# Kernel tuning notes

Hardware: AMD Instinct MI355X
Metric: run time of the kernel (lower is better)

Reference implementation:

```python
import jax, jax.numpy as jnp
import numpy as np

B, N, K, D, H, L = 2, 2048, 256, 768, 150, 11
REL_PROP = 2
NB = 10  # distance buckets


def _lin(key, din, dout):
    return jax.random.normal(key, (din, dout), dtype=jnp.float32) / np.sqrt(din)


def setup_inputs() -> dict:
    key = jax.random.key(0)
    ks = jax.random.split(key, 16)
    rng = np.random.default_rng(0)
    prune_idx = jnp.asarray(np.stack([np.sort(rng.permutation(N)[:K]) for _ in range(B)]), dtype=jnp.int32)
    span_begin = jnp.sort(jax.random.randint(ks[2], (B, K), 0, N - 16), axis=-1).astype(jnp.int32)
    span_end = (span_begin + jax.random.randint(ks[3], (B, K), 1, 16)).astype(jnp.int32)
    return {
        "all_span_vecs": jax.random.normal(ks[0], (B, N, D), dtype=jnp.float32),
        "update": jax.random.normal(ks[1], (B, K, D), dtype=jnp.float32),
        "square_mask": jnp.ones((B, K, K), dtype=jnp.float32),
        "span_lengths": jnp.full((B,), float(K), dtype=jnp.float32),
        "span_begin": span_begin,
        "span_end": span_end,
        "prune_indices": prune_idx,
        "w_left": _lin(ks[4], D, H), "b_left": jnp.zeros((H,), jnp.float32),
        "w_right": _lin(ks[5], D, H), "b_right": jnp.zeros((H,), jnp.float32),
        "dist_emb": jax.random.normal(ks[6], (NB, H), dtype=jnp.float32) * 0.02,
        "w_h": _lin(ks[7], H, H), "b_h": jnp.zeros((H,), jnp.float32),
        "w_out": _lin(ks[8], H, L), "b_out": jnp.zeros((L,), jnp.float32),
        "a_w": _lin(ks[9], L, D),
        "gate_w": _lin(ks[10], 2 * D, D), "gate_b": jnp.zeros((D,), jnp.float32),
        "pr_w": _lin(ks[11], D, 1), "pr_b": jnp.zeros((1,), jnp.float32),
    }


def _pair_scores(u, bins, w_left, b_left, w_right, b_right, dist_emb, w_h, b_h, w_out, b_out):
    # OptFFpairs: left/right span projections + pairwise distance embedding -> FF -> L labels
    left = u @ w_left + b_left          # [B,K,H]
    right = u @ w_right + b_right       # [B,K,H]
    h = jax.nn.relu(left[:, :, None, :] + right[:, None, :, :] + dist_emb[bins])  # [B,K,K,H]
    h = jax.nn.relu(h @ w_h + b_h)
    return h @ w_out + b_out            # [B,K,K,L]


def _add_unary(rel, ss):
    # relation_add_scores: add per-span pruner scores along both pair axes; ss: [B,K,1]
    return rel + ss[:, :, None, :] + ss[:, None, :, :]


def reference(all_span_vecs, update, square_mask, span_lengths, span_begin, span_end,
              prune_indices, w_left, b_left, w_right, b_right, dist_emb, w_h, b_h,
              w_out, b_out, a_w, gate_w, gate_b, pr_w, pr_b):
    bins = jnp.clip(jnp.abs(span_begin[:, None, :] - span_begin[:, :, None]), 0, NB - 1)  # [B,K,K]
    rel = _pair_scores(update, bins, w_left, b_left, w_right, b_right, dist_emb, w_h, b_h, w_out, b_out)
    rel = _add_unary(rel, update @ pr_w + pr_b)
    for _ in range(REL_PROP):
        probs = jax.nn.relu(rel) * square_mask[..., None]     # [B,K,K,L]
        msg = probs @ a_w                                     # A(probs): [B,K,K,D]
        # ctxt[b,j,d] = sum_i msg[b,i,j,d] * update[b,i,d] / span_lengths[b]
        ctxt = (msg * update[:, :, None, :]).sum(-3) / span_lengths[:, None, None]
        g = jax.nn.sigmoid(jnp.concatenate([update, ctxt], axis=-1) @ gate_w + gate_b)
        update = g * update + (1.0 - g) * ctxt                # MyGate
        rel = _pair_scores(update, bins, w_left, b_left, w_right, b_right, dist_emb, w_h, b_h, w_out, b_out)
        rel = _add_unary(rel, update @ pr_w + pr_b)           # pruner.scorer(update)
    # overwrite_spans: scatter updated filtered spans back into the full span tensor
    valid = jnp.arange(K)[None, :] < span_lengths[:, None]    # [B,K]
    bidx = jnp.arange(B)[:, None]
    orig = all_span_vecs[bidx, prune_indices]                 # [B,K,D]
    vals = jnp.where(valid[..., None], update, orig)
    update_all = all_span_vecs.at[bidx, prune_indices].set(vals)
    return update_all, update, rel
```

## Files before the change

kernel.cpp:

```cpp
#include <hip/hip_runtime.h>
#include <hip/hip_bf16.h>
#include <math.h>

#define BB 2
#define NN 2048
#define KK 256
#define DD 768
#define HH 150
#define LL 11
#define NBINS 10

#define KP 160
#define WP 40
#define GWP 136
#define BPAD 264

typedef __attribute__((ext_vector_type(8))) short short8;
typedef __attribute__((ext_vector_type(4))) short s16x4;
typedef __attribute__((ext_vector_type(4))) float f32x4;

__device__ inline unsigned bf2u(float lo, float hi) {
  union { __hip_bfloat162 b; unsigned u; } cv;
  cv.b = __float22bfloat162_rn(make_float2(lo, hi));
  return cv.u;
}
__device__ inline short bf1(float x) {
  union { __hip_bfloat16 b; short s; } cv;
  cv.b = __float2bfloat16(x);
  return cv.s;
}
__device__ inline float ubf(short b) {
  return __uint_as_float(((unsigned)(unsigned short)b) << 16);
}

#define PRE_PREP 110
#define PRE_CVT  1536
#define PRE_TRGW 1152
#define PRE_TRWLR 240
#define PRE_TRUPD 384
#define PRE_NB (PRE_PREP + PRE_CVT + PRE_TRGW + PRE_TRWLR + PRE_TRUPD)

__global__ __launch_bounds__(256) void k_pre(
    const float* __restrict__ w_h, const float* __restrict__ w_out,
    short* __restrict__ wt, short* __restrict__ wo,
    const float* __restrict__ upd_in, short* __restrict__ updbf,
    const float* __restrict__ gate_w, short* __restrict__ gwt,
    const float* __restrict__ w_left, const float* __restrict__ w_right,
    short* __restrict__ wlrt, short* __restrict__ updT)
{
  __shared__ float tile[32][33];
  int bid = blockIdx.x;
  int t = threadIdx.x;

  if (bid < PRE_PREP) {
    int idx = bid * 256 + t;
    if (idx < KP * KP) {
      int n = idx / KP, k = idx - n * KP;
      float v = (n < HH && k < HH) ? w_h[k * HH + n] : 0.f;
      wt[idx] = bf1(v);
    }
    int idx2 = idx - KP * KP;
    if (idx2 >= 0 && idx2 < 16 * KP) {
      int n = idx2 / KP, k = idx2 - n * KP;
      float v = (n < LL && k < HH) ? w_out[k * LL + n] : 0.f;
      wo[idx2] = bf1(v);
    }
    return;
  }
  bid -= PRE_PREP;
  if (bid < PRE_CVT) {
    int idx = bid * 256 + t;
    if (idx < BB * KK * DD) updbf[idx] = bf1(upd_in[idx]);
    return;
  }
  bid -= PRE_CVT;
  if (bid < PRE_TRGW) {
    int kt = bid % 48, nt = bid / 48;
    int m0 = kt * 32, n0 = nt * 32;
    int tx = t & 31, ty = t >> 5;
    #pragma unroll
    for (int r = 0; r < 4; ++r)
      tile[ty + r * 8][tx] = gate_w[(size_t)(m0 + ty + r * 8) * DD + n0 + tx];
    __syncthreads();
    #pragma unroll
    for (int r = 0; r < 4; ++r)
      gwt[(size_t)(n0 + ty + r * 8) * (2 * DD) + m0 + tx] = bf1(tile[tx][ty + r * 8]);
    return;
  }
  bid -= PRE_TRGW;
  if (bid < PRE_TRWLR) {
    int kt = bid % 24, nt = bid / 24;
    int k0 = kt * 32, n0 = nt * 32;
    const float* src = (n0 >= KP) ? w_right : w_left;
    int col0 = n0 - (n0 >= KP ? KP : 0);
    int tx = t & 31, ty = t >> 5;
    #pragma unroll
    for (int r = 0; r < 4; ++r) {
      int col = col0 + tx;
      tile[ty + r * 8][tx] = (col < HH) ? src[(size_t)(k0 + ty + r * 8) * HH + col] : 0.f;
    }
    __syncthreads();
    #pragma unroll
    for (int r = 0; r < 4; ++r)
      wlrt[(size_t)(n0 + ty + r * 8) * DD + k0 + tx] = bf1(tile[tx][ty + r * 8]);
    return;
  }
  bid -= PRE_TRWLR;
  {
    int b = bid / 192;
    int r = bid - b * 192;
    int it = r & 7, dt = r >> 3;
    int i0 = it * 32, d0 = dt * 32;
    int tx = t & 31, ty = t >> 5;
    #pragma unroll
    for (int rr = 0; rr < 4; ++rr)
      tile[ty + rr * 8][tx] = upd_in[(size_t)(b * KK + i0 + ty + rr * 8) * DD + d0 + tx];
    __syncthreads();
    #pragma unroll
    for (int rr = 0; rr < 4; ++rr)
      updT[(size_t)(b * DD + d0 + ty + rr * 8) * KK + i0 + tx] = bf1(tile[tx][ty + rr * 8]);
  }
}

__global__ __launch_bounds__(256) void k_projss(
    const short* __restrict__ updbf, const short* __restrict__ wlrt,
    const float* __restrict__ b_left, const float* __restrict__ b_right,
    const float* __restrict__ updf, const float* __restrict__ pr_w,
    const float* __restrict__ pr_b,
    float* __restrict__ left, float* __restrict__ right, float* __restrict__ ssv)
{
  __shared__ short As[64][WP];
  __shared__ short Bs[KP][WP];
  int bidx = blockIdx.x;
  int t = threadIdx.x;

  if (bidx >= 16) {
    int row = (bidx - 16) * 4 + (t >> 6);
    int l = t & 63;
    float s = 0.f;
    for (int d = l; d < DD; d += 64) s = fmaf(updf[(size_t)row * DD + d], pr_w[d], s);
    #pragma unroll
    for (int off = 32; off > 0; off >>= 1) s += __shfl_down(s, off);
    if (l == 0) ssv[row] = s + pr_b[0];
    return;
  }

  int rbk = bidx >> 1, half = bidx & 1;
  int row0 = rbk * 64;
  const short* wsrc = wlrt + (size_t)half * KP * DD;
  int l = t & 63, w = t >> 6, lr = l & 15, lg = l >> 4;
  int ar = t >> 2, ac = t & 3;
  int i1 = t + 256, i2 = t + 512;
  f32x4 acc[10];
  #pragma unroll
  for (int nt = 0; nt < 10; ++nt) acc[nt] = (f32x4){0.f, 0.f, 0.f, 0.f};

  short8 pa, pb0, pb1, pb2 = {};
  pa  = *(const short8*)(updbf + (size_t)(row0 + ar) * DD + ac * 8);
  pb0 = *(const short8*)(wsrc + (size_t)(t >> 2) * DD + (t & 3) * 8);
  pb1 = *(const short8*)(wsrc + (size_t)(i1 >> 2) * DD + (i1 & 3) * 8);
  if (i2 < 640) pb2 = *(const short8*)(wsrc + (size_t)(i2 >> 2) * DD + (i2 & 3) * 8);

  for (int ks = 0; ks < 24; ++ks) {
    __syncthreads();
    *(short8*)&As[ar][ac * 8] = pa;
    *(short8*)&Bs[t >> 2][(t & 3) * 8] = pb0;
    *(short8*)&Bs[i1 >> 2][(i1 & 3) * 8] = pb1;
    if (i2 < 640) *(short8*)&Bs[i2 >> 2][(i2 & 3) * 8] = pb2;
    __syncthreads();
    if (ks + 1 < 24) {
      int k0 = (ks + 1) * 32;
      pa  = *(const short8*)(updbf + (size_t)(row0 + ar) * DD + k0 + ac * 8);
      pb0 = *(const short8*)(wsrc + (size_t)(t >> 2) * DD + k0 + (t & 3) * 8);
      pb1 = *(const short8*)(wsrc + (size_t)(i1 >> 2) * DD + k0 + (i1 & 3) * 8);
      if (i2 < 640) pb2 = *(const short8*)(wsrc + (size_t)(i2 >> 2) * DD + k0 + (i2 & 3) * 8);
    }
    short8 a = *(short8*)&As[w * 16 + lr][lg * 8];
    #pragma unroll
    for (int nt = 0; nt < 10; ++nt) {
      short8 b = *(short8*)&Bs[nt * 16 + lr][lg * 8];
      acc[nt] = __builtin_amdgcn_mfma_f32_16x16x32_bf16(a, b, acc[nt], 0, 0, 0);
    }
  }
  const float* bias = half ? b_right : b_left;
  float* dst = half ? right : left;
  int rowb = row0 + w * 16 + lg * 4;
  #pragma unroll
  for (int nt = 0; nt < 10; ++nt) {
    int col = nt * 16 + lr;
    if (col < HH) {
      float bv = bias[col];
      #pragma unroll
      for (int q = 0; q < 4; ++q)
        dst[(size_t)(rowb + q) * HH + col] = acc[nt][q] + bv;
    }
  }
}

template <bool WPT>
__global__ __launch_bounds__(256, 4) void k_pair_mfma(
    const float* __restrict__ left, const float* __restrict__ right,
    const float* __restrict__ ss, const int* __restrict__ span_begin,
    const float* __restrict__ demb,
    const short* __restrict__ wt, const short* __restrict__ wo,
    const float* __restrict__ b_h, const float* __restrict__ b_out,
    const float* __restrict__ mask,
    float* __restrict__ rel, short* __restrict__ probsT)
{
  int bid = blockIdx.x;
  int b  = bid >> 10;
  int r2 = bid & 1023;
  int i  = r2 >> 2;
  int j0 = (r2 & 3) * 64;

  __shared__ short wtbuf[2][32 * KP];
  __shared__ float ld_s[NBINS][KP];
  __shared__ float bh_s[KP];
  __shared__ float ssj_s[64];
  __shared__ float m_s[64];
  __shared__ int   bins[64];

  int t = threadIdx.x;
  int l = t & 63, w = t >> 6;
  int lr = l & 15, lg = l >> 4;

  int sbi = span_begin[b * KK + i];
  if (t < 64) {
    int d = span_begin[b * KK + j0 + t] - sbi; d = d < 0 ? -d : d;
    bins[t] = d > NBINS - 1 ? NBINS - 1 : d;
    ssj_s[t] = ss[b * KK + j0 + t];
    if (WPT) m_s[t] = mask[((size_t)(b * KK + i)) * KK + j0 + t];
  }
  for (int idx = t; idx < KP; idx += 256) bh_s[idx] = (idx < HH) ? b_h[idx] : 0.f;
  {
    const float* lrow = left + (size_t)(b * KK + i) * HH;
    for (int idx = t; idx < NBINS * KP; idx += 256) {
      int bn = idx / KP, k = idx - bn * KP;
      ld_s[bn][k] = (k < HH) ? (lrow[k] + demb[bn * HH + k]) : 0.f;
    }
  }
  short8 wo_f[5];
  #pragma unroll
  for (int ks = 0; ks < 5; ++ks)
    wo_f[ks] = *(const short8*)(wo + lr * KP + ks * 32 + lg * 8);

  short8 pw[3];
  #pragma unroll
  for (int c = 0; c < 3; ++c) {
    int idx = t + c * 256;
    if (idx < 640) pw[c] = *(const short8*)(wt + idx * 8);
  }
  #pragma unroll
  for (int c = 0; c < 3; ++c) {
    int idx = t + c * 256;
    if (idx < 640) *(short8*)&wtbuf[0][idx * 8] = pw[c];
  }
  #pragma unroll
  for (int c = 0; c < 3; ++c) {
    int idx = t + c * 256;
    if (idx < 640) pw[c] = *(const short8*)(wt + 5120 + idx * 8);
  }
  __syncthreads();

  int jr = w * 16 + lr;
  int binr = bins[jr];
  const float* rrow = right + (size_t)(b * KK + j0 + jr) * HH;
  const float* ldr = &ld_s[binr][0];
  short8 afr[5];
  #pragma unroll
  for (int ks = 0; ks < 5; ++ks) {
    unsigned pk[4];
    #pragma unroll
    for (int e = 0; e < 4; ++e) {
      int k = ks * 32 + lg * 8 + e * 2;
      float2 r2v = (k < HH - 1) ? *(const float2*)(rrow + k) : make_float2(0.f, 0.f);
      float2 lv = *(const float2*)(ldr + k);
      float v0 = fmaxf(lv.x + r2v.x, 0.f);
      float v1 = fmaxf(lv.y + r2v.y, 0.f);
      pk[e] = bf2u(v0, v1);
    }
    int4 tmp; tmp.x = (int)pk[0]; tmp.y = (int)pk[1]; tmp.z = (int)pk[2]; tmp.w = (int)pk[3];
    afr[ks] = *(short8*)&tmp;
  }

  f32x4 acc[10];
  #pragma unroll
  for (int m = 0; m < 10; ++m) acc[m] = (f32x4){0.f, 0.f, 0.f, 0.f};

  #pragma unroll
  for (int s = 0; s < 5; ++s) {
    if (s > 0) __syncthreads();
    if (s + 1 < 5) {
      #pragma unroll
      for (int c = 0; c < 3; ++c) {
        int idx = t + c * 256;
        if (idx < 640) *(short8*)&wtbuf[(s + 1) & 1][idx * 8] = pw[c];
      }
      if (s + 2 < 5) {
        #pragma unroll
        for (int c = 0; c < 3; ++c) {
          int idx = t + c * 256;
          if (idx < 640) pw[c] = *(const short8*)(wt + (s + 2) * 5120 + idx * 8);
        }
      }
    }
    const short* bufp = &wtbuf[s & 1][0];
    #pragma unroll
    for (int ks = 0; ks < 5; ++ks) {
      short8 a = afr[ks];
      #pragma unroll
      for (int ntp = 0; ntp < 2; ++ntp) {
        short8 bf = *(const short8*)(bufp + (ntp * 16 + lr) * KP + ks * 32 + lg * 8);
        acc[s * 2 + ntp] = __builtin_amdgcn_mfma_f32_16x16x32_bf16(a, bf, acc[s * 2 + ntp], 0, 0, 0);
      }
    }
  }
  __syncthreads();

  short* h1 = &wtbuf[0][0];
  #pragma unroll
  for (int m = 0; m < 10; ++m) {
    int col = (m >> 1) * 32 + (m & 1) * 16 + lr;
    float bh = bh_s[col];
    #pragma unroll
    for (int q = 0; q < 4; ++q) {
      int row = w * 16 + lg * 4 + q;
      h1[row * KP + col] = bf1(fmaxf(acc[m][q] + bh, 0.f));
    }
  }
  __syncthreads();

  f32x4 acc2 = (f32x4){0.f, 0.f, 0.f, 0.f};
  #pragma unroll
  for (int ks = 0; ks < 5; ++ks) {
    short8 a = *(const short8*)(h1 + (w * 16 + lr) * KP + ks * 32 + lg * 8);
    acc2 = __builtin_amdgcn_mfma_f32_16x16x32_bf16(a, wo_f[ks], acc2, 0, 0, 0);
  }

  float ssi = ss[b * KK + i];
  float* out_s = (float*)&ld_s[0][0];
  if (lr < LL) {
    float bo = b_out[lr];
    #pragma unroll
    for (int q = 0; q < 4; ++q) {
      int row = w * 16 + lg * 4 + q;
      out_s[row * 12 + lr] = acc2[q] + bo + ssi + ssj_s[row];
    }
  }
  __syncthreads();
  size_t base = ((size_t)(b * KK + i) * KK + j0) * LL;
  for (int idx = t; idx < 64 * LL; idx += 256) {
    int j = idx / LL, ll2 = idx - j * LL;
    rel[base + idx] = out_s[j * 12 + ll2];
  }
  if (WPT) {
    for (int idx = t; idx < 64 * LL; idx += 256) {
      int j = idx / LL, ll2 = idx - j * LL;
      float v = fmaxf(out_s[j * 12 + ll2], 0.f) * m_s[j];
      probsT[(((size_t)(b * LL + ll2)) * KK + j0 + j) * KK + i] = bf1(v);
    }
  }
}

__global__ __launch_bounds__(256) void k_ctxt_mfma(
    const short* __restrict__ probsT, const short* __restrict__ updT,
    const float* __restrict__ a_w, const float* __restrict__ span_len,
    short* __restrict__ ctxbf)
{
  int bidx = blockIdx.x;
  int b = bidx / 96;
  int r = bidx - b * 96;
  int jt = r / 12, dt = r - jt * 12;
  int j0 = jt * 32, d0 = dt * 64;

  __shared__ short Bs[64][BPAD];
  __shared__ short As[32][BPAD];

  int t = threadIdx.x, l = t & 63, w = t >> 6, lr = l & 15, lg = l >> 4;
  int wr = w >> 1, wc = w & 1;

  for (int s = 0; s < 8; ++s) {
    int idx = t + s * 256;
    int row = idx >> 5, c = idx & 31;
    *(short8*)&Bs[row][c * 8] =
        *(const short8*)(updT + ((size_t)(b * DD + d0 + row)) * KK + c * 8);
  }

  short8 pa[4];
  #pragma unroll
  for (int s = 0; s < 4; ++s) {
    int idx = t + s * 256;
    int row = idx >> 5, c = idx & 31;
    pa[s] = *(const short8*)(probsT + (((size_t)(b * LL + 0)) * KK + j0 + row) * KK + c * 8);
  }

  f32x4 accF[2];
  accF[0] = (f32x4){0.f, 0.f, 0.f, 0.f};
  accF[1] = (f32x4){0.f, 0.f, 0.f, 0.f};

  for (int ll = 0; ll < LL; ++ll) {
    __syncthreads();
    #pragma unroll
    for (int s = 0; s < 4; ++s) {
      int idx = t + s * 256;
      int row = idx >> 5, c = idx & 31;
      *(short8*)&As[row][c * 8] = pa[s];
    }
    if (ll + 1 < LL) {
      #pragma unroll
      for (int s = 0; s < 4; ++s) {
        int idx = t + s * 256;
        int row = idx >> 5, c = idx & 31;
        pa[s] = *(const short8*)(probsT + (((size_t)(b * LL + ll + 1)) * KK + j0 + row) * KK + c * 8);
      }
    }
    float awl[2];
    #pragma unroll
    for (int nt = 0; nt < 2; ++nt) awl[nt] = a_w[ll * DD + d0 + wc * 32 + nt * 16 + lr];
    __syncthreads();

    f32x4 accL[2];
    accL[0] = (f32x4){0.f, 0.f, 0.f, 0.f};
    accL[1] = (f32x4){0.f, 0.f, 0.f, 0.f};
    #pragma unroll
    for (int ks = 0; ks < 8; ++ks) {
      short8 a = *(short8*)&As[wr * 16 + lr][ks * 32 + lg * 8];
      #pragma unroll
      for (int nt = 0; nt < 2; ++nt) {
        short8 bf = *(short8*)&Bs[wc * 32 + nt * 16 + lr][ks * 32 + lg * 8];
        accL[nt] = __builtin_amdgcn_mfma_f32_16x16x32_bf16(a, bf, accL[nt], 0, 0, 0);
      }
    }
    #pragma unroll
    for (int nt = 0; nt < 2; ++nt)
      #pragma unroll
      for (int q = 0; q < 4; ++q)
        accF[nt][q] = fmaf(awl[nt], accL[nt][q], accF[nt][q]);
  }

  float inv = 1.f / span_len[b];
  int rowb = j0 + wr * 16 + lg * 4;
  #pragma unroll
  for (int nt = 0; nt < 2; ++nt) {
    int col = d0 + wc * 32 + nt * 16 + lr;
    #pragma unroll
    for (int q = 0; q < 4; ++q) {
      size_t off = (size_t)(b * KK + rowb + q) * DD + col;
      ctxbf[off] = bf1(accF[nt][q] * inv);
    }
  }
}

template <bool LAST>
__global__ __launch_bounds__(256) void k_gate_mfma(
    const short* __restrict__ updbf, const short* __restrict__ ctxbf,
    const short* __restrict__ gwt, const float* __restrict__ gate_b,
    const float* __restrict__ updr, float* __restrict__ updw,
    short* __restrict__ nxtbf, short* __restrict__ updT,
    const int* __restrict__ prune, const float* __restrict__ span_len,
    float* __restrict__ out_all)
{
  int rb = blockIdx.x / 12, cb = blockIdx.x - rb * 12;
  int row0 = rb * 32, col0 = cb * 64;
  __shared__ short As[32][GWP];
  __shared__ short Bs[64][GWP];
  int t = threadIdx.x, l = t & 63, w = t >> 6, lr = l & 15, lg = l >> 4;
  int wr = w >> 1, wc = w & 1;

  f32x4 acc[2];
  acc[0] = (f32x4){0.f, 0.f, 0.f, 0.f};
  acc[1] = (f32x4){0.f, 0.f, 0.f, 0.f};

  short8 pa[2], pb[4];
  #pragma unroll
  for (int s = 0; s < 2; ++s) {
    int idx = t + s * 256;
    pa[s] = *(const short8*)(updbf + (size_t)(row0 + (idx >> 4)) * DD + (idx & 15) * 8);
  }
  #pragma unroll
  for (int s = 0; s < 4; ++s) {
    int idx = t + s * 256;
    pb[s] = *(const short8*)(gwt + (size_t)(col0 + (idx >> 4)) * (2 * DD) + (idx & 15) * 8);
  }

  for (int ph = 0; ph < 12; ++ph) {
    __syncthreads();
    #pragma unroll
    for (int s = 0; s < 2; ++s) {
      int idx = t + s * 256;
      *(short8*)&As[idx >> 4][(idx & 15) * 8] = pa[s];
    }
    #pragma unroll
    for (int s = 0; s < 4; ++s) {
      int idx = t + s * 256;
      *(short8*)&Bs[idx >> 4][(idx & 15) * 8] = pb[s];
    }
    if (ph + 1 < 12) {
      int k0 = (ph + 1) * 128;
      #pragma unroll
      for (int s = 0; s < 2; ++s) {
        int idx = t + s * 256;
        int ka = k0 + (idx & 15) * 8;
        const short* asrc = (ka < DD) ? (updbf + (size_t)(row0 + (idx >> 4)) * DD + ka)
                                      : (ctxbf + (size_t)(row0 + (idx >> 4)) * DD + ka - DD);
        pa[s] = *(const short8*)asrc;
      }
      #pragma unroll
      for (int s = 0; s < 4; ++s) {
        int idx = t + s * 256;
        pb[s] = *(const short8*)(gwt + (size_t)(col0 + (idx >> 4)) * (2 * DD) + k0 + (idx & 15) * 8);
      }
    }
    __syncthreads();
    #pragma unroll
    for (int ksub = 0; ksub < 4; ++ksub) {
      short8 a = *(short8*)&As[wr * 16 + lr][ksub * 32 + lg * 8];
      #pragma unroll
      for (int nt = 0; nt < 2; ++nt) {
        short8 bf = *(short8*)&Bs[wc * 32 + nt * 16 + lr][ksub * 32 + lg * 8];
        acc[nt] = __builtin_amdgcn_mfma_f32_16x16x32_bf16(a, bf, acc[nt], 0, 0, 0);
      }
    }
  }
  int rowb = row0 + wr * 16 + lg * 4;
  int bb = rowb >> 8, ii = rowb & 255;
  #pragma unroll
  for (int nt = 0; nt < 2; ++nt) {
    int col = col0 + wc * 32 + nt * 16 + lr;
    float gb = gate_b[col];
    s16x4 tw;
    #pragma unroll
    for (int q = 0; q < 4; ++q) {
      size_t off = (size_t)(rowb + q) * DD + col;
      float x = acc[nt][q] + gb;
      float g = 1.f / (1.f + expf(-x));
      float cv = ubf(ctxbf[off]);
      float o = g * updr[off] + (1.f - g) * cv;
      updw[off] = o;
      short bv = bf1(o);
      nxtbf[off] = bv;
      tw[q] = bv;
      if (LAST) {
        int iq = ii + q;
        if ((float)iq < span_len[bb]) {
          int dst = prune[bb * KK + iq];
          out_all[((size_t)(bb * NN + dst)) * DD + col] = o;
        }
      }
    }
    *(s16x4*)(updT + ((size_t)(bb * DD + col)) * KK + ii) = tw;
  }
}

extern "C" void kernel_launch(void* const* d_in, const int* in_sizes, int n_in,
                              void* d_out, int out_size, void* d_ws, size_t ws_size,
                              hipStream_t stream)
{
  (void)in_sizes; (void)n_in; (void)out_size; (void)ws_size;
  const float* all_span = (const float*)d_in[0];
  const float* upd_in   = (const float*)d_in[1];
  const float* mask     = (const float*)d_in[2];
  const float* span_len = (const float*)d_in[3];
  const int*   span_beg = (const int*)d_in[4];
  const int*   prune    = (const int*)d_in[6];
  const float* w_left   = (const float*)d_in[7];
  const float* b_left   = (const float*)d_in[8];
  const float* w_right  = (const float*)d_in[9];
  const float* b_right  = (const float*)d_in[10];
  const float* dist_emb = (const float*)d_in[11];
  const float* w_h      = (const float*)d_in[12];
  const float* b_h      = (const float*)d_in[13];
  const float* w_out    = (const float*)d_in[14];
  const float* b_out    = (const float*)d_in[15];
  const float* a_w      = (const float*)d_in[16];
  const float* gate_w   = (const float*)d_in[17];
  const float* gate_b   = (const float*)d_in[18];
  const float* pr_w     = (const float*)d_in[19];
  const float* pr_b     = (const float*)d_in[20];

  float* out_all = (float*)d_out;
  float* out_upd = out_all + (size_t)BB * NN * DD;
  float* out_rel = out_upd + (size_t)BB * KK * DD;

  float* ws     = (float*)d_ws;
  float* left   = ws;
  float* right  = left + (size_t)BB * KK * HH;
  float* ssv    = right + (size_t)BB * KK * HH + 64;
  short* wt_bf  = (short*)(ssv + (size_t)BB * KK);
  short* wo_bf  = wt_bf + KP * KP;
  short* updbf0 = wo_bf + 16 * KP;
  short* updbf1 = updbf0 + (size_t)BB * KK * DD;
  short* ctxbf  = updbf1 + (size_t)BB * KK * DD;
  short* gwt    = ctxbf + (size_t)BB * KK * DD;
  short* wlrt   = gwt + (size_t)DD * 2 * DD;
  short* probsT = wlrt + (size_t)2 * KP * DD;
  short* updT   = probsT + (size_t)BB * LL * KK * KK;

  hipMemcpyAsync(out_all, all_span, sizeof(float) * (size_t)BB * NN * DD,
                 hipMemcpyDeviceToDevice, stream);
  k_pre<<<PRE_NB, 256, 0, stream>>>(w_h, w_out, wt_bf, wo_bf, upd_in, updbf0,
                                    gate_w, gwt, w_left, w_right, wlrt, updT);

  k_projss<<<144, 256, 0, stream>>>(updbf0, wlrt, b_left, b_right, upd_in,
                                    pr_w, pr_b, left, right, ssv);
  k_pair_mfma<true><<<BB * KK * 4, 256, 0, stream>>>(
      left, right, ssv, span_beg, dist_emb, wt_bf, wo_bf, b_h, b_out, mask,
      out_rel, probsT);

  for (int p = 0; p < 2; ++p) {
    short* cur_bf = (p == 0) ? updbf0 : updbf1;
    short* nxt_bf = (p == 0) ? updbf1 : updbf0;
    const float* updr = (p == 0) ? upd_in : out_upd;
    k_ctxt_mfma<<<BB * 8 * 12, 256, 0, stream>>>(probsT, updT, a_w, span_len, ctxbf);
    if (p == 0) {
      k_gate_mfma<false><<<16 * 12, 256, 0, stream>>>(
          cur_bf, ctxbf, gwt, gate_b, updr, out_upd, nxt_bf, updT,
          prune, span_len, out_all);
    } else {
      k_gate_mfma<true><<<16 * 12, 256, 0, stream>>>(
          cur_bf, ctxbf, gwt, gate_b, updr, out_upd, nxt_bf, updT,
          prune, span_len, out_all);
    }
    k_projss<<<144, 256, 0, stream>>>(nxt_bf, wlrt, b_left, b_right, out_upd,
                                      pr_w, pr_b, left, right, ssv);
    if (p == 0) {
      k_pair_mfma<true><<<BB * KK * 4, 256, 0, stream>>>(
          left, right, ssv, span_beg, dist_emb, wt_bf, wo_bf, b_h, b_out, mask,
          out_rel, probsT);
    } else {
      k_pair_mfma<false><<<BB * KK * 4, 256, 0, stream>>>(
          left, right, ssv, span_beg, dist_emb, wt_bf, wo_bf, b_h, b_out, mask,
          out_rel, probsT);
    }
  }
}
```

Baseline: 190.7 us.

## Vectorize bf16 convert, skip dead rel writes, halve ctxt tile width

```diff
diff --git a/kernel.cpp b/kernel.cpp
--- a/kernel.cpp
+++ b/kernel.cpp
@@ -34,7 +34,7 @@
 }
 
 #define PRE_PREP 110
-#define PRE_CVT  1536
+#define PRE_CVT  192
 #define PRE_TRGW 1152
 #define PRE_TRWLR 240
 #define PRE_TRUPD 384
@@ -69,8 +69,15 @@
   }
   bid -= PRE_PREP;
   if (bid < PRE_CVT) {
-    int idx = bid * 256 + t;
-    if (idx < BB * KK * DD) updbf[idx] = bf1(upd_in[idx]);
+    int idx = (bid * 256 + t) * 8;
+    const float4* s4 = (const float4*)(upd_in + idx);
+    float4 a = s4[0], c = s4[1];
+    int4 pk;
+    pk.x = (int)bf2u(a.x, a.y);
+    pk.y = (int)bf2u(a.z, a.w);
+    pk.z = (int)bf2u(c.x, c.y);
+    pk.w = (int)bf2u(c.z, c.w);
+    *(int4*)(updbf + idx) = pk;
     return;
   }
   bid -= PRE_CVT;
@@ -348,12 +355,13 @@
     }
   }
   __syncthreads();
-  size_t base = ((size_t)(b * KK + i) * KK + j0) * LL;
-  for (int idx = t; idx < 64 * LL; idx += 256) {
-    int j = idx / LL, ll2 = idx - j * LL;
-    rel[base + idx] = out_s[j * 12 + ll2];
-  }
-  if (WPT) {
+  if (!WPT) {
+    size_t base = ((size_t)(b * KK + i) * KK + j0) * LL;
+    for (int idx = t; idx < 64 * LL; idx += 256) {
+      int j = idx / LL, ll2 = idx - j * LL;
+      rel[base + idx] = out_s[j * 12 + ll2];
+    }
+  } else {
     for (int idx = t; idx < 64 * LL; idx += 256) {
       int j = idx / LL, ll2 = idx - j * LL;
       float v = fmaxf(out_s[j * 12 + ll2], 0.f) * m_s[j];
@@ -368,18 +376,18 @@
     short* __restrict__ ctxbf)
 {
   int bidx = blockIdx.x;
-  int b = bidx / 96;
-  int r = bidx - b * 96;
-  int jt = r / 12, dt = r - jt * 12;
-  int j0 = jt * 32, d0 = dt * 64;
-
-  __shared__ short Bs[64][BPAD];
+  int b = bidx / 192;
+  int r = bidx - b * 192;
+  int jt = r / 24, dt = r - jt * 24;
+  int j0 = jt * 32, d0 = dt * 32;
+
+  __shared__ short Bs[32][BPAD];
   __shared__ short As[32][BPAD];
 
   int t = threadIdx.x, l = t & 63, w = t >> 6, lr = l & 15, lg = l >> 4;
   int wr = w >> 1, wc = w & 1;
 
-  for (int s = 0; s < 8; ++s) {
+  for (int s = 0; s < 4; ++s) {
     int idx = t + s * 256;
     int row = idx >> 5, c = idx & 31;
     *(short8*)&Bs[row][c * 8] =
@@ -394,9 +402,7 @@
     pa[s] = *(const short8*)(probsT + (((size_t)(b * LL + 0)) * KK + j0 + row) * KK + c * 8);
   }
 
-  f32x4 accF[2];
-  accF[0] = (f32x4){0.f, 0.f, 0.f, 0.f};
-  accF[1] = (f32x4){0.f, 0.f, 0.f, 0.f};
+  f32x4 accF = (f32x4){0.f, 0.f, 0.f, 0.f};
 
   for (int ll = 0; ll < LL; ++ll) {
     __syncthreads();
@@ -414,40 +420,28 @@
         pa[s] = *(const short8*)(probsT + (((size_t)(b * LL + ll + 1)) * KK + j0 + row) * KK + c * 8);
       }
     }
-    float awl[2];
-    #pragma unroll
-    for (int nt = 0; nt < 2; ++nt) awl[nt] = a_w[ll * DD + d0 + wc * 32 + nt * 16 + lr];
-    __syncthreads();
-
-    f32x4 accL[2];
-    accL[0] = (f32x4){0.f, 0.f, 0.f, 0.f};
-    accL[1] = (f32x4){0.f, 0.f, 0.f, 0.f};
+    float awl = a_w[ll * DD + d0 + wc * 16 + lr];
+    __syncthreads();
+
+    f32x4 accL = (f32x4){0.f, 0.f, 0.f, 0.f};
     #pragma unroll
     for (int ks = 0; ks < 8; ++ks) {
       short8 a = *(short8*)&As[wr * 16 + lr][ks * 32 + lg * 8];
-      #pragma unroll
-      for (int nt = 0; nt < 2; ++nt) {
-        short8 bf = *(short8*)&Bs[wc * 32 + nt * 16 + lr][ks * 32 + lg * 8];
-        accL[nt] = __builtin_amdgcn_mfma_f32_16x16x32_bf16(a, bf, accL[nt], 0, 0, 0);
-      }
-    }
-    #pragma unroll
-    for (int nt = 0; nt < 2; ++nt)
-      #pragma unroll
-      for (int q = 0; q < 4; ++q)
-        accF[nt][q] = fmaf(awl[nt], accL[nt][q], accF[nt][q]);
+      short8 bf = *(short8*)&Bs[wc * 16 + lr][ks * 32 + lg * 8];
+      accL = __builtin_amdgcn_mfma_f32_16x16x32_bf16(a, bf, accL, 0, 0, 0);
+    }
+    #pragma unroll
+    for (int q = 0; q < 4; ++q)
+      accF[q] = fmaf(awl, accL[q], accF[q]);
   }
 
   float inv = 1.f / span_len[b];
   int rowb = j0 + wr * 16 + lg * 4;
-  #pragma unroll
-  for (int nt = 0; nt < 2; ++nt) {
-    int col = d0 + wc * 32 + nt * 16 + lr;
-    #pragma unroll
-    for (int q = 0; q < 4; ++q) {
-      size_t off = (size_t)(b * KK + rowb + q) * DD + col;
-      ctxbf[off] = bf1(accF[nt][q] * inv);
-    }
+  int col = d0 + wc * 16 + lr;
+  #pragma unroll
+  for (int q = 0; q < 4; ++q) {
+    size_t off = (size_t)(b * KK + rowb + q) * DD + col;
+    ctxbf[off] = bf1(accF[q] * inv);
   }
 }
 
@@ -611,7 +605,7 @@
     short* cur_bf = (p == 0) ? updbf0 : updbf1;
     short* nxt_bf = (p == 0) ? updbf1 : updbf0;
     const float* updr = (p == 0) ? upd_in : out_upd;
-    k_ctxt_mfma<<<BB * 8 * 12, 256, 0, stream>>>(probsT, updT, a_w, span_len, ctxbf);
+    k_ctxt_mfma<<<BB * 8 * 24, 256, 0, stream>>>(probsT, updT, a_w, span_len, ctxbf);
     if (p == 0) {
       k_gate_mfma<false><<<16 * 12, 256, 0, stream>>>(
           cur_bf, ctxbf, gwt, gate_b, updr, out_upd, nxt_bf, updT,
```

After: 190.3 us. Within noise of the previous version (-0.2%).
